# Optimization experiments

Measured on AMD Instinct MI355X. Metric: run time of the kernel, lower is better.

Reference implementation:

```python
import jax, jax.numpy as jnp
import numpy as np
from jax import lax

N = 1024          # n_ligand == n_receptor == feature dim (required by broadcast in source)
D = 1024          # gnn_input_dim == gnn_output_dim
H = 32            # hopi_output_dim
C = 32            # cnn_channels


def setup_inputs() -> dict:
    key = jax.random.key(0)
    ks = jax.random.split(key, 24)
    s = 0.02
    inp = {
        "ligand_node_features": jax.random.normal(ks[0], (N, D), jnp.float32),
        "ligand_edge_features": jax.random.normal(ks[1], (N, D), jnp.float32),
        "ligand_adjacency": jax.random.uniform(ks[2], (N, N), jnp.float32),
        "receptor_node_features": jax.random.normal(ks[3], (N, D), jnp.float32),
        "receptor_edge_features": jax.random.normal(ks[4], (N, D), jnp.float32),
        "receptor_adjacency": jax.random.uniform(ks[5], (N, N), jnp.float32),
        # GNNLayer params (shared between ligand and receptor, as in source)
        "Wn": jax.random.normal(ks[6], (D, D), jnp.float32) * s,
        "bn": jax.random.normal(ks[7], (D,), jnp.float32) * s,
        "We": jax.random.normal(ks[8], (D, D), jnp.float32) * s,
        "be": jax.random.normal(ks[9], (D,), jnp.float32) * s,
        "Wa": jax.random.normal(ks[10], (1, D), jnp.float32) * s,
        "ba": jax.random.normal(ks[11], (1,), jnp.float32) * s,
        # HighOrderPairwiseInteraction: Linear(2*D -> H)
        "W_hopi": jax.random.normal(ks[12], (H, 2 * D), jnp.float32) * s,
        "b_hopi": jax.random.normal(ks[13], (H,), jnp.float32) * s,
        # CNN tail
        "conv1_w": jax.random.normal(ks[14], (C, H, 3, 3), jnp.float32) * s,
        "conv1_b": jax.random.normal(ks[15], (C,), jnp.float32) * s,
        "conv2_w": jax.random.normal(ks[16], (C, C, 3, 3), jnp.float32) * s,
        "conv2_b": jax.random.normal(ks[17], (C,), jnp.float32) * s,
        "conv3_w": jax.random.normal(ks[18], (1, C, 1, 1), jnp.float32) * s,
        "conv3_b": jax.random.normal(ks[19], (1,), jnp.float32) * s,
    }
    return inp


def _gnn(nf, ef, Wn, bn, We, be, Wa, ba):
    # aggregated: [N, D]
    agg = jnp.tanh(nf @ Wn.T + bn + ef @ We.T + be)
    scores = agg @ Wa.T + ba                      # [N, 1]
    attn = jax.nn.softmax(scores, axis=1)         # softmax over size-1 dim -> ones (faithful)
    weighted = jnp.sum(agg * attn, axis=1)        # [N]
    return nf + weighted                          # [N,D] + [N] broadcasts over last dim (D == N)


def _conv(x, w, b):
    y = lax.conv_general_dilated(x, w, (1, 1), "SAME",
                                 dimension_numbers=("NCHW", "OIHW", "NCHW"))
    return y + b[None, :, None, None]


def reference(ligand_node_features, ligand_edge_features, ligand_adjacency,
              receptor_node_features, receptor_edge_features, receptor_adjacency,
              Wn, bn, We, be, Wa, ba, W_hopi, b_hopi,
              conv1_w, conv1_b, conv2_w, conv2_b, conv3_w, conv3_b):
    lig = _gnn(ligand_node_features, ligand_edge_features, Wn, bn, We, be, Wa, ba)
    rec = _gnn(receptor_node_features, receptor_edge_features, Wn, bn, We, be, Wa, ba)

    # HOPI: interactions[i, j] = Linear(cat(lig[i], rec[j])) == lig[i] @ Wl.T + rec[j] @ Wr.T + b
    Wl, Wr = W_hopi[:, :D], W_hopi[:, D:]
    lig_p = lig @ Wl.T                            # [N, H]
    rec_p = rec @ Wr.T                            # [N, H]
    interactions = lig_p[:, None, :] + rec_p[None, :, :] + b_hopi  # [N, N, H]

    x = jnp.transpose(interactions, (2, 0, 1))[None]  # [1, H, N, N]
    x = jax.nn.relu(_conv(x, conv1_w, conv1_b))
    x = jax.nn.relu(_conv(x, conv2_w, conv2_b))
    x = _conv(x, conv3_w, conv3_b)                # [1, 1, N, N]
    return x[0, 0]                                # [N, N]
```

## Files before the change

kernel.cpp:

```cpp
#include <hip/hip_runtime.h>


typedef _Float16 half8 __attribute__((ext_vector_type(8)));
typedef _Float16 half4 __attribute__((ext_vector_type(4)));
typedef float    f32x4 __attribute__((ext_vector_type(4)));

__device__ __forceinline__ short f2h_bits(float f){
    _Float16 h = (_Float16)f;
    return __builtin_bit_cast(short, h);
}
__device__ __forceinline__ half8 pack2(const float4& x, const float4& y){
    half8 r;
    r[0] = (_Float16)x.x; r[1] = (_Float16)x.y;
    r[2] = (_Float16)x.z; r[3] = (_Float16)x.w;
    r[4] = (_Float16)y.x; r[5] = (_Float16)y.y;
    r[6] = (_Float16)y.z; r[7] = (_Float16)y.w;
    return r;
}
__device__ __forceinline__ float tanh_fast(float x){
    float e = __expf(2.f * x);
    return 1.f - 2.f / (e + 1.f);
}

#define SWZ(c) ((((c) >> 1) & 3) << 3)

#define GNN_LOAD(AV, BV, KBN) {                                              \
    const int kbn_ = (KBN) & 2047;                                           \
    const float* Asrc_ = (kbn_ < 1024) ? A0 : A1;                            \
    const float* Bsrc_ = (kbn_ < 1024) ? Wn : We;                            \
    const int kk_ = kbn_ & 1023;                                             \
    const float* ap_ = Asrc_ + (size_t)(j0 + arow) * 1024 + kk_ + akc;       \
    const float* bp_ = Bsrc_ + (size_t)(d0 + brow) * 1024 + kk_ + bkc;       \
    AV[0] = *reinterpret_cast<const float4*>(ap_);                           \
    AV[1] = *reinterpret_cast<const float4*>(ap_ + 4);                       \
    AV[2] = *reinterpret_cast<const float4*>(ap_ + 8);                       \
    AV[3] = *reinterpret_cast<const float4*>(ap_ + 12);                      \
    BV[0] = *reinterpret_cast<const float4*>(bp_);                           \
    BV[1] = *reinterpret_cast<const float4*>(bp_ + 4);                       \
}

#define GNN_STAGE(AV, BV) {                                                  \
    const int ga_ = (t & 3) * 2;                                             \
    const int sa_ = arow & 7;                                                \
    *reinterpret_cast<half8*>(&As[arow * 64 + ((ga_    ) ^ sa_) * 8]) = pack2(AV[0], AV[1]); \
    *reinterpret_cast<half8*>(&As[arow * 64 + ((ga_ + 1) ^ sa_) * 8]) = pack2(AV[2], AV[3]); \
    *reinterpret_cast<half8*>(&Bs[brow * 64 + ((t & 7) ^ (brow & 7)) * 8]) = pack2(BV[0], BV[1]); \
}

#define GNN_MFMA() {                                                         \
    _Pragma("unroll")                                                        \
    for (int ks = 0; ks < 2; ++ks){                                          \
        half8 Af[2], Bf[2];                                                  \
        _Pragma("unroll")                                                    \
        for (int m = 0; m < 2; ++m){                                         \
            int row = wm * 32 + m * 16 + lr;                                 \
            int g   = ((ks * 4 + lg) ^ (row & 7)) * 8;                       \
            Af[m] = *reinterpret_cast<const half8*>(&As[row * 64 + g]);      \
        }                                                                    \
        _Pragma("unroll")                                                    \
        for (int n = 0; n < 2; ++n){                                         \
            int col = wn * 32 + n * 16 + lr;                                 \
            int g   = ((ks * 4 + lg) ^ (col & 7)) * 8;                       \
            Bf[n] = *reinterpret_cast<const half8*>(&Bs[col * 64 + g]);      \
        }                                                                    \
        _Pragma("unroll")                                                    \
        for (int m = 0; m < 2; ++m)                                          \
            _Pragma("unroll")                                                \
            for (int n = 0; n < 2; ++n)                                      \
                acc[m][n] = __builtin_amdgcn_mfma_f32_16x16x32_f16(          \
                    Af[m], Bf[n], acc[m][n], 0, 0, 0);                       \
    }                                                                        \
}

__global__ __launch_bounds__(512) void gnn_kernel(
    const float* __restrict__ lig_nf, const float* __restrict__ lig_ef,
    const float* __restrict__ rec_nf, const float* __restrict__ rec_ef,
    const float* __restrict__ Wn, const float* __restrict__ We,
    const float* __restrict__ bn, const float* __restrict__ be,
    float* __restrict__ part)
{
    __shared__ __attribute__((aligned(16))) short As[128 * 64];
    __shared__ __attribute__((aligned(16))) short Bs[64 * 64];
    __shared__ float red[128][2];

    const int t  = threadIdx.x;
    const int cx = blockIdx.z;
    const float* A0 = cx ? rec_nf : lig_nf;
    const float* A1 = cx ? rec_ef : lig_ef;
    const int j0 = blockIdx.x * 128;
    const int d0 = blockIdx.y * 64;

    const int wid  = t >> 6;
    const int wm   = wid >> 1;
    const int wn   = wid & 1;
    const int lane = t & 63;
    const int lr   = lane & 15;
    const int lg   = lane >> 4;

    f32x4 acc[2][2];
    #pragma unroll
    for (int m = 0; m < 2; ++m)
        #pragma unroll
        for (int n = 0; n < 2; ++n)
            acc[m][n] = (f32x4){0.f, 0.f, 0.f, 0.f};

    const int arow = t >> 2;
    const int akc  = (t & 3) * 16;
    const int brow = t >> 3;
    const int bkc  = (t & 7) * 8;

    float4 avA[4], bvA[2], avB[4], bvB[2];
    GNN_LOAD(avA, bvA, 0);
    GNN_LOAD(avB, bvB, 64);

    for (int kb = 0; kb < 2048; kb += 128){
        __syncthreads();
        GNN_STAGE(avA, bvA);
        GNN_LOAD(avA, bvA, kb + 128);
        __syncthreads();
        GNN_MFMA();
        __syncthreads();
        GNN_STAGE(avB, bvB);
        GNN_LOAD(avB, bvB, kb + 192);
        __syncthreads();
        GNN_MFMA();
    }

    float rowsum[2][4];
    #pragma unroll
    for (int m = 0; m < 2; ++m)
        #pragma unroll
        for (int jj = 0; jj < 4; ++jj) rowsum[m][jj] = 0.f;
    #pragma unroll
    for (int n = 0; n < 2; ++n){
        int d = d0 + wn * 32 + n * 16 + lr;
        float bias = bn[d] + be[d];
        #pragma unroll
        for (int m = 0; m < 2; ++m)
            #pragma unroll
            for (int jj = 0; jj < 4; ++jj)
                rowsum[m][jj] += tanh_fast(acc[m][n][jj] + bias);
    }
    #pragma unroll
    for (int mask = 1; mask < 16; mask <<= 1)
        #pragma unroll
        for (int m = 0; m < 2; ++m)
            #pragma unroll
            for (int jj = 0; jj < 4; ++jj)
                rowsum[m][jj] += __shfl_xor(rowsum[m][jj], mask);
    __syncthreads();
    if (lr == 0){
        #pragma unroll
        for (int m = 0; m < 2; ++m)
            #pragma unroll
            for (int jj = 0; jj < 4; ++jj)
                red[wm * 32 + m * 16 + lg * 4 + jj][wn] = rowsum[m][jj];
    }
    __syncthreads();
    if (t < 128)
        part[(size_t)cx * 16384 + (size_t)blockIdx.y * 1024 + j0 + t]
            = red[t][0] + red[t][1];
}

__global__ __launch_bounds__(256) void pp_kernel(
    const float* __restrict__ lig_nf, const float* __restrict__ rec_nf,
    const float* __restrict__ W_hopi, const float* __restrict__ b_hopi,
    const float* __restrict__ w1, const float* __restrict__ b1,
    const float* __restrict__ w2,
    const float* __restrict__ part,
    float* __restrict__ Kp, short* __restrict__ U16, short* __restrict__ V16,
    short* __restrict__ w2f16)
{
    __shared__ __attribute__((aligned(16))) char smem[46208];
    const int t = threadIdx.x;
    const int role = blockIdx.x;

    if (role < 32){
        short* As = reinterpret_cast<short*>(smem);
        short* Bs = reinterpret_cast<short*>(smem + 10240);
        short* Pz = reinterpret_cast<short*>(smem + 14336);
        short* Ws = reinterpret_cast<short*>(smem + 20736);

        const int cx = role >> 4;
        const int r0 = (role & 15) * 64;
        const float* nf = cx ? rec_nf : lig_nf;
        const float* W  = W_hopi + (cx ? 1024 : 0);
        short* O = cx ? V16 : U16;

        const int wid = t >> 6;
        const int lane = t & 63;
        const int lr = lane & 15;
        const int lg = lane >> 4;

        for (int e = t; e < 9216; e += 256){
            int cs  = e / 3072;
            int rem = e - cs * 3072;
            int co  = rem / 96;
            int k   = rem - co * 96;
            int d   = k >> 5;
            int ci  = k & 31;
            int o_lo = (cs == 1) ? 1 : 0;
            int o_hi = (cs == 2) ? 1 : 2;
            float s = 0.f;
            for (int o = o_lo; o <= o_hi; ++o){
                int tap = cx ? (o * 3 + d) : (d * 3 + o);
                s += w1[co * 288 + ci * 9 + tap];
            }
            Ws[(cs * 32 + co) * 104 + k] = f2h_bits(s);
        }

        f32x4 acc[2][2];
        #pragma unroll
        for (int mi = 0; mi < 2; ++mi)
            #pragma unroll
            for (int n = 0; n < 2; ++n)
                acc[mi][n] = (f32x4){0.f, 0.f, 0.f, 0.f};

        for (int kb = 0; kb < 16; ++kb){
            const int kcol = kb * 64;
            __syncthreads();
            for (int e = t; e < 320; e += 256){
                int rowl = e >> 2;
                int grow = r0 - 8 + rowl;
                int chunk = (e & 3) * 16;
                float4 a0, a1, a2, a3;
                if ((unsigned)grow < 1024u){
                    const float* ap = nf + (size_t)grow * 1024 + kcol + chunk;
                    a0 = *reinterpret_cast<const float4*>(ap);
                    a1 = *reinterpret_cast<const float4*>(ap + 4);
                    a2 = *reinterpret_cast<const float4*>(ap + 8);
                    a3 = *reinterpret_cast<const float4*>(ap + 12);
                } else {
                    a0 = a1 = a2 = a3 = make_float4(0.f, 0.f, 0.f, 0.f);
                }
                int ga = (e & 3) * 2;
                int sa = rowl & 7;
                *reinterpret_cast<half8*>(&As[rowl * 64 + ((ga    ) ^ sa) * 8]) = pack2(a0, a1);
                *reinterpret_cast<half8*>(&As[rowl * 64 + ((ga + 1) ^ sa) * 8]) = pack2(a2, a3);
            }
            {
                int row = t >> 3;
                int kc  = (t & 7) * 8;
                const float* bp = W + (size_t)row * 2048 + kcol + kc;
                float4 b0 = *reinterpret_cast<const float4*>(bp);
                float4 b1 = *reinterpret_cast<const float4*>(bp + 4);
                *reinterpret_cast<half8*>(&Bs[row * 64 + ((t & 7) ^ (row & 7)) * 8]) = pack2(b0, b1);
            }
            __syncthreads();
            #pragma unroll
            for (int mi = 0; mi < 2; ++mi){
                int mf = wid + mi * 4;
                if (mf >= 5) break;
                #pragma unroll
                for (int ks = 0; ks < 2; ++ks){
                    int ar = mf * 16 + lr;
                    half8 Af = *reinterpret_cast<const half8*>(
                        &As[ar * 64 + ((ks * 4 + lg) ^ (ar & 7)) * 8]);
                    #pragma unroll
                    for (int n = 0; n < 2; ++n){
                        int col = n * 16 + lr;
                        half8 Bf = *reinterpret_cast<const half8*>(
                            &Bs[col * 64 + ((ks * 4 + lg) ^ (col & 7)) * 8]);
                        acc[mi][n] = __builtin_amdgcn_mfma_f32_16x16x32_f16(
                            Af, Bf, acc[mi][n], 0, 0, 0);
                    }
                }
            }
        }
        #pragma unroll
        for (int mi = 0; mi < 2; ++mi){
            int mf = wid + mi * 4;
            if (mf >= 5) break;
            #pragma unroll
            for (int n = 0; n < 2; ++n)
                #pragma unroll
                for (int jj = 0; jj < 4; ++jj){
                    int rowl = mf * 16 + lg * 4 + jj;
                    Pz[rowl * 40 + n * 16 + lr] = f2h_bits(acc[mi][n][jj]);
                }
        }
        __syncthreads();

        f32x4 uacc[3][2];
        #pragma unroll
        for (int cs = 0; cs < 3; ++cs)
            #pragma unroll
            for (int n = 0; n < 2; ++n)
                uacc[cs][n] = (f32x4){0.f, 0.f, 0.f, 0.f};
        #pragma unroll
        for (int d = 0; d < 3; ++d){
            int ar = wid * 16 + lr;
            half8 Ap = *reinterpret_cast<const half8*>(
                &Pz[(7 + ar + d) * 40 + lg * 8]);
            #pragma unroll
            for (int cs = 0; cs < 3; ++cs)
                #pragma unroll
                for (int n = 0; n < 2; ++n){
                    half8 Bp = *reinterpret_cast<const half8*>(
                        &Ws[(cs * 32 + n * 16 + lr) * 104 + d * 32 + lg * 8]);
                    uacc[cs][n] = __builtin_amdgcn_mfma_f32_16x16x32_f16(
                        Ap, Bp, uacc[cs][n], 0, 0, 0);
                }
        }
        #pragma unroll
        for (int cs = 0; cs < 3; ++cs)
            #pragma unroll
            for (int n = 0; n < 2; ++n)
                #pragma unroll
                for (int jj = 0; jj < 4; ++jj){
                    int grow = r0 + wid * 16 + lg * 4 + jj;
                    O[((size_t)(cs << 10) + grow) * 32 + n * 16 + lr]
                        = f2h_bits(uacc[cs][n][jj]);
                }
        return;
    }

    if (role == 33){
        for (int e = t; e < 9216; e += 256){
            int co  = e / 288;
            int rem = e - co * 288;
            int ci  = rem / 9;
            int tap = rem - ci * 9;
            w2f16[(tap * 32 + co) * 32 + (ci ^ SWZ(co))] = f2h_bits(w2[e]);
        }
        return;
    }

    float* ws_l = reinterpret_cast<float*>(smem);
    float* ws_r = reinterpret_cast<float*>(smem + 4096);
    float* red  = reinterpret_cast<float*>(smem + 8192);
    float* cvs  = reinterpret_cast<float*>(smem + 9216);
    float* w1s  = reinterpret_cast<float*>(smem + 9344);

    #pragma unroll
    for (int q = 0; q < 9; ++q){
        int idx = (t + q * 256) * 4;
        *reinterpret_cast<float4*>(&w1s[idx]) =
            *reinterpret_cast<const float4*>(w1 + idx);
    }
    for (int j = t; j < 1024; j += 256){
        float sl = 0.f, sr = 0.f;
        #pragma unroll
        for (int b = 0; b < 16; ++b){
            sl += part[b * 1024 + j];
            sr += part[16384 + b * 1024 + j];
        }
        ws_l[j] = sl; ws_r[j] = sr;
    }
    __syncthreads();
    {
        const int h = t & 31;
        const int seg = t >> 5;
        const float* wl = W_hopi + (size_t)h * 2048 + seg * 128;
        const float* wr = wl + 1024;
        float s = 0.f;
        #pragma unroll 8
        for (int j = 0; j < 128; j += 4){
            float4 a = *reinterpret_cast<const float4*>(wl + j);
            float4 b = *reinterpret_cast<const float4*>(wr + j);
            const float* l = &ws_l[seg * 128 + j];
            const float* r = &ws_r[seg * 128 + j];
            s = fmaf(l[0], a.x, s); s = fmaf(l[1], a.y, s);
            s = fmaf(l[2], a.z, s); s = fmaf(l[3], a.w, s);
            s = fmaf(r[0], b.x, s); s = fmaf(r[1], b.y, s);
            s = fmaf(r[2], b.z, s); s = fmaf(r[3], b.w, s);
        }
        red[t] = s;
    }
    __syncthreads();
    if (t < 32){
        float tot = b_hopi[t];
        #pragma unroll
        for (int g = 0; g < 8; ++g) tot += red[g * 32 + t];
        cvs[t] = tot;
    }
    __syncthreads();
    for (int e = t; e < 288; e += 256){
        int co  = e & 31;
        int cse = e >> 5;
        int yc  = cse / 3, xc = cse - yc * 3;
        float sum = b1[co];
        for (int ci = 0; ci < 32; ++ci){
            const float* wp = &w1s[co * 288 + ci * 9];
            float t00 = wp[0], t01 = wp[1], t02 = wp[2];
            float t10 = wp[3], t11 = wp[4], t12 = wp[5];
            float t20 = wp[6], t21 = wp[7], t22 = wp[8];
            float r0, r1, r2;
            if (xc == 0){ r0 = t00+t01+t02; r1 = t10+t11+t12; r2 = t20+t21+t22; }
            else if (xc == 1){ r0 = t01+t02; r1 = t11+t12; r2 = t21+t22; }
            else { r0 = t00+t01; r1 = t10+t11; r2 = t20+t21; }
            float wsum = (yc == 0) ? (r0+r1+r2) : ((yc == 1) ? (r1+r2) : (r0+r1));
            sum = fmaf(cvs[ci], wsum, sum);
        }
        Kp[cse * 32 + co] = sum;
    }
}

__global__ __launch_bounds__(512) void conv_kernel(
    const short* __restrict__ U16, const short* __restrict__ V16,
    const float* __restrict__ Kp, const short* __restrict__ w2f16,
    const float* __restrict__ b2,
    const float* __restrict__ w3, const float* __restrict__ b3,
    float* __restrict__ outp)
{
    __shared__ __attribute__((aligned(16))) short ys[18 * 18 * 32];
    __shared__ __attribute__((aligned(16))) short wB[9 * 32 * 32];

    const int t    = threadIdx.x;
    const int oy0  = blockIdx.y * 16;
    const int ox0  = blockIdx.x * 16;
    const int wid  = t >> 6;
    const int lane = t & 63;
    const int lr   = lane & 15;
    const int lg   = lane >> 4;

    {
        const uint4* src = reinterpret_cast<const uint4*>(w2f16);
        uint4* dst = reinterpret_cast<uint4*>(wB);
        #pragma unroll
        for (int e = t; e < 1152; e += 512)
            dst[e] = src[e];
    }
    const bool interior = (blockIdx.x >= 1) & (blockIdx.x <= 62) &
                          (blockIdx.y >= 1) & (blockIdx.y <= 62);
    if (interior){
        const int cp = (t & 7) * 4;
        half4 k00;
        {
            float4 kf = *reinterpret_cast<const float4*>(&Kp[cp]);
            k00[0] = (_Float16)kf.x; k00[1] = (_Float16)kf.y;
            k00[2] = (_Float16)kf.z; k00[3] = (_Float16)kf.w;
        }
        #pragma unroll
        for (int pass = 0; pass < 6; ++pass){
            int idx = t + pass * 512;
            if (idx < 2592){
                int po  = idx >> 3;
                int ryo = po / 18;
                int rxo = po - ryo * 18;
                int gy = oy0 - 1 + ryo, gx = ox0 - 1 + rxo;
                half4 u = *reinterpret_cast<const half4*>(&U16[gy * 32 + cp]);
                half4 v = *reinterpret_cast<const half4*>(&V16[gx * 32 + cp]);
                half4 r = u + v + k00;
                #pragma unroll
                for (int e = 0; e < 4; ++e)
                    r[e] = r[e] > (_Float16)0.f ? r[e] : (_Float16)0.f;
                *reinterpret_cast<half4*>(&ys[po * 32 + (cp ^ SWZ(rxo))]) = r;
            }
        }
    } else {
        #pragma unroll
        for (int pass = 0; pass < 6; ++pass){
            int idx = t + pass * 512;
            if (idx < 2592){
                int po  = idx >> 3;
                int cp  = (idx & 7) * 4;
                int ryo = po / 18;
                int rxo = po - ryo * 18;
                int gy = oy0 - 1 + ryo, gx = ox0 - 1 + rxo;
                half4 h = {(_Float16)0.f, (_Float16)0.f, (_Float16)0.f, (_Float16)0.f};
                if ((unsigned)gy < 1024u && (unsigned)gx < 1024u){
                    int yc = (gy == 0) ? 1 : ((gy == 1023) ? 2 : 0);
                    int xc = (gx == 0) ? 1 : ((gx == 1023) ? 2 : 0);
                    half4 u = *reinterpret_cast<const half4*>(
                        &U16[((size_t)(xc << 10) + gy) * 32 + cp]);
                    half4 v = *reinterpret_cast<const half4*>(
                        &V16[((size_t)(yc << 10) + gx) * 32 + cp]);
                    float4 k = *reinterpret_cast<const float4*>(&Kp[(yc * 3 + xc) * 32 + cp]);
                    h[0] = (_Float16)fmaxf((float)u[0] + (float)v[0] + k.x, 0.f);
                    h[1] = (_Float16)fmaxf((float)u[1] + (float)v[1] + k.y, 0.f);
                    h[2] = (_Float16)fmaxf((float)u[2] + (float)v[2] + k.z, 0.f);
                    h[3] = (_Float16)fmaxf((float)u[3] + (float)v[3] + k.w, 0.f);
                }
                *reinterpret_cast<half4*>(&ys[po * 32 + (cp ^ SWZ(rxo))]) = h;
            }
        }
    }
    __syncthreads();

    {
        half8 Bf[2][9];
        float bias[2], w3v[2];
        #pragma unroll
        for (int n = 0; n < 2; ++n){
            int co = n * 16 + lr;
            bias[n] = b2[co];
            w3v[n]  = w3[co];
            #pragma unroll
            for (int tap = 0; tap < 9; ++tap)
                Bf[n][tap] = *reinterpret_cast<const half8*>(
                    &wB[(tap * 32 + co) * 32 + ((lg * 8) ^ SWZ(co))]);
        }
        const float b3v = b3[0];
        for (int s = wid; s < 16; s += 8){
            int p  = s * 16 + lr;
            int ry = p >> 4;
            int rx = p & 15;
            f32x4 acc0 = {0.f, 0.f, 0.f, 0.f};
            f32x4 acc1 = {0.f, 0.f, 0.f, 0.f};
            #pragma unroll
            for (int tap = 0; tap < 9; ++tap){
                const int dy = tap / 3, dx = tap - (tap / 3) * 3;
                int pix = (ry + dy) * 18 + rx + dx;
                half8 A = *reinterpret_cast<const half8*>(
                    &ys[pix * 32 + ((lg * 8) ^ SWZ(rx + dx))]);
                acc0 = __builtin_amdgcn_mfma_f32_16x16x32_f16(A, Bf[0][tap], acc0, 0, 0, 0);
                acc1 = __builtin_amdgcn_mfma_f32_16x16x32_f16(A, Bf[1][tap], acc1, 0, 0, 0);
            }
            float part[4];
            #pragma unroll
            for (int j = 0; j < 4; ++j)
                part[j] = w3v[0] * fmaxf(acc0[j] + bias[0], 0.f)
                        + w3v[1] * fmaxf(acc1[j] + bias[1], 0.f);
            #pragma unroll
            for (int m = 1; m < 16; m <<= 1)
                #pragma unroll
                for (int j = 0; j < 4; ++j)
                    part[j] += __shfl_xor(part[j], m);
            if (lr == 0){
                float4 o = make_float4(part[0] + b3v, part[1] + b3v,
                                       part[2] + b3v, part[3] + b3v);
                *reinterpret_cast<float4*>(outp + (size_t)(oy0 + s) * 1024 + ox0 + lg * 4) = o;
            }
        }
    }
}

extern "C" void kernel_launch(void* const* d_in, const int* in_sizes, int n_in,
                              void* d_out, int out_size, void* d_ws, size_t ws_size,
                              hipStream_t stream)
{
    const float* lig_nf = (const float*)d_in[0];
    const float* lig_ef = (const float*)d_in[1];
    const float* rec_nf = (const float*)d_in[3];
    const float* rec_ef = (const float*)d_in[4];
    const float* Wn     = (const float*)d_in[6];
    const float* bn     = (const float*)d_in[7];
    const float* We     = (const float*)d_in[8];
    const float* be     = (const float*)d_in[9];
    const float* W_hopi = (const float*)d_in[12];
    const float* b_hopi = (const float*)d_in[13];
    const float* w1     = (const float*)d_in[14];
    const float* b1     = (const float*)d_in[15];
    const float* w2     = (const float*)d_in[16];
    const float* b2     = (const float*)d_in[17];
    const float* w3     = (const float*)d_in[18];
    const float* b3     = (const float*)d_in[19];
    float* outp = (float*)d_out;

    float* part  = (float*)d_ws;
    float* Kp    = (float*)((char*)d_ws + 393216);
    short* U16   = (short*)((char*)d_ws + 394368);
    short* V16   = (short*)((char*)d_ws + 590976);
    short* w2f16 = (short*)((char*)d_ws + 787584);

    dim3 g1(8, 16, 2);
    gnn_kernel<<<g1, 512, 0, stream>>>(lig_nf, lig_ef, rec_nf, rec_ef,
                                       Wn, We, bn, be, part);
    pp_kernel<<<34, 256, 0, stream>>>(lig_nf, rec_nf, W_hopi, b_hopi,
                                      w1, b1, w2, part, Kp, U16, V16, w2f16);
    dim3 g3(64, 64);
    conv_kernel<<<g3, 512, 0, stream>>>(U16, V16, Kp, w2f16, b2, w3, b3, outp);
}
```

Baseline: 117.9 us.

## Double-buffer register prefetch in pp_kernel and widen blocks to 512 threads

Rewrites the HOPI projection GEMM in pp_kernel so global loads for the next two K-tiles go into registers while the current tile is staged to LDS and multiplied. The block grows from 256 to 512 threads so each of 5 waves owns one 16-row M fragment instead of waves looping over two. The other roles are adjusted for the new thread count. This aims to hide global load latency in a small 34-block kernel, at the cost of more registers and extra barriers per K step.

New measurement: 114.9 us. 2.5% less time.

```diff
diff --git a/kernel.cpp b/kernel.cpp
--- a/kernel.cpp
+++ b/kernel.cpp
@@ -15,6 +15,12 @@
     r[2] = (_Float16)x.z; r[3] = (_Float16)x.w;
     r[4] = (_Float16)y.x; r[5] = (_Float16)y.y;
     r[6] = (_Float16)y.z; r[7] = (_Float16)y.w;
+    return r;
+}
+__device__ __forceinline__ half4 pack4(const float4& x){
+    half4 r;
+    r[0] = (_Float16)x.x; r[1] = (_Float16)x.y;
+    r[2] = (_Float16)x.z; r[3] = (_Float16)x.w;
     return r;
 }
 __device__ __forceinline__ float tanh_fast(float x){
@@ -162,7 +168,66 @@
             = red[t][0] + red[t][1];
 }
 
-__global__ __launch_bounds__(256) void pp_kernel(
+#define PP_LOAD(AV, BV, KBN) {                                               \
+    const int kcol_ = (KBN) & 1023;                                          \
+    _Pragma("unroll")                                                        \
+    for (int p = 0; p < 3; ++p){                                             \
+        int e_ = t + 512 * p;                                                \
+        if (e_ < 1280){                                                      \
+            int rowl_ = e_ >> 4;                                             \
+            int grow_ = r0 - 8 + rowl_;                                      \
+            if ((unsigned)grow_ < 1024u)                                     \
+                AV[p] = *reinterpret_cast<const float4*>(                    \
+                    nf + (size_t)grow_ * 1024 + kcol_ + (e_ & 15) * 4);      \
+            else                                                             \
+                AV[p] = make_float4(0.f, 0.f, 0.f, 0.f);                     \
+        }                                                                    \
+    }                                                                        \
+    BV = *reinterpret_cast<const float4*>(                                   \
+        W + (size_t)(t >> 4) * 2048 + kcol_ + (t & 15) * 4);                 \
+}
+
+#define PP_STAGE(AV, BV) {                                                   \
+    _Pragma("unroll")                                                        \
+    for (int p = 0; p < 3; ++p){                                             \
+        int e_ = t + 512 * p;                                                \
+        if (e_ < 1280){                                                      \
+            int rowl_ = e_ >> 4;                                             \
+            int ga_ = (e_ & 15) >> 1;                                        \
+            int sub_ = (e_ & 1) * 4;                                         \
+            *reinterpret_cast<half4*>(                                       \
+                &As[rowl_ * 64 + ((ga_ ^ (rowl_ & 7)) * 8) + sub_]) = pack4(AV[p]); \
+        }                                                                    \
+    }                                                                        \
+    {                                                                        \
+        int row_ = t >> 4;                                                   \
+        int ga_ = (t & 15) >> 1;                                             \
+        int sub_ = (t & 1) * 4;                                              \
+        *reinterpret_cast<half4*>(                                           \
+            &Bs[row_ * 64 + ((ga_ ^ (row_ & 7)) * 8) + sub_]) = pack4(BV);   \
+    }                                                                        \
+}
+
+#define PP_MFMA() {                                                          \
+    if (wid < 5){                                                            \
+        _Pragma("unroll")                                                    \
+        for (int ks = 0; ks < 2; ++ks){                                      \
+            int ar_ = wid * 16 + lr;                                         \
+            half8 Af = *reinterpret_cast<const half8*>(                      \
+                &As[ar_ * 64 + ((ks * 4 + lg) ^ (ar_ & 7)) * 8]);            \
+            _Pragma("unroll")                                                \
+            for (int n = 0; n < 2; ++n){                                     \
+                int col_ = n * 16 + lr;                                      \
+                half8 Bf = *reinterpret_cast<const half8*>(                  \
+                    &Bs[col_ * 64 + ((ks * 4 + lg) ^ (col_ & 7)) * 8]);      \
+                pacc[n] = __builtin_amdgcn_mfma_f32_16x16x32_f16(            \
+                    Af, Bf, pacc[n], 0, 0, 0);                               \
+            }                                                                \
+        }                                                                    \
+    }                                                                        \
+}
+
+__global__ __launch_bounds__(512) void pp_kernel(
     const float* __restrict__ lig_nf, const float* __restrict__ rec_nf,
     const float* __restrict__ W_hopi, const float* __restrict__ b_hopi,
     const float* __restrict__ w1, const float* __restrict__ b1,
@@ -171,7 +236,7 @@
     float* __restrict__ Kp, short* __restrict__ U16, short* __restrict__ V16,
     short* __restrict__ w2f16)
 {
-    __shared__ __attribute__((aligned(16))) char smem[46208];
+    __shared__ __attribute__((aligned(16))) char smem[47232];
     const int t = threadIdx.x;
     const int role = blockIdx.x;
 
@@ -192,7 +257,7 @@
         const int lr = lane & 15;
         const int lg = lane >> 4;
 
-        for (int e = t; e < 9216; e += 256){
+        for (int e = t; e < 9216; e += 512){
             int cs  = e / 3072;
             int rem = e - cs * 3072;
             int co  = rem / 96;
@@ -209,114 +274,77 @@
             Ws[(cs * 32 + co) * 104 + k] = f2h_bits(s);
         }
 
-        f32x4 acc[2][2];
-        #pragma unroll
-        for (int mi = 0; mi < 2; ++mi)
-            #pragma unroll
-            for (int n = 0; n < 2; ++n)
-                acc[mi][n] = (f32x4){0.f, 0.f, 0.f, 0.f};
-
-        for (int kb = 0; kb < 16; ++kb){
-            const int kcol = kb * 64;
+        f32x4 pacc[2];
+        pacc[0] = (f32x4){0.f, 0.f, 0.f, 0.f};
+        pacc[1] = (f32x4){0.f, 0.f, 0.f, 0.f};
+
+        float4 avA[3], avB[3];
+        float4 bvA, bvB;
+        PP_LOAD(avA, bvA, 0);
+        PP_LOAD(avB, bvB, 64);
+
+        for (int kb = 0; kb < 1024; kb += 128){
             __syncthreads();
-            for (int e = t; e < 320; e += 256){
-                int rowl = e >> 2;
-                int grow = r0 - 8 + rowl;
-                int chunk = (e & 3) * 16;
-                float4 a0, a1, a2, a3;
-                if ((unsigned)grow < 1024u){
-                    const float* ap = nf + (size_t)grow * 1024 + kcol + chunk;
-                    a0 = *reinterpret_cast<const float4*>(ap);
-                    a1 = *reinterpret_cast<const float4*>(ap + 4);
-                    a2 = *reinterpret_cast<const float4*>(ap + 8);
-                    a3 = *reinterpret_cast<const float4*>(ap + 12);
-                } else {
-                    a0 = a1 = a2 = a3 = make_float4(0.f, 0.f, 0.f, 0.f);
-                }
-                int ga = (e & 3) * 2;
-                int sa = rowl & 7;
-                *reinterpret_cast<half8*>(&As[rowl * 64 + ((ga    ) ^ sa) * 8]) = pack2(a0, a1);
-                *reinterpret_cast<half8*>(&As[rowl * 64 + ((ga + 1) ^ sa) * 8]) = pack2(a2, a3);
-            }
-            {
-                int row = t >> 3;
-                int kc  = (t & 7) * 8;
-                const float* bp = W + (size_t)row * 2048 + kcol + kc;
-                float4 b0 = *reinterpret_cast<const float4*>(bp);
-                float4 b1 = *reinterpret_cast<const float4*>(bp + 4);
-                *reinterpret_cast<half8*>(&Bs[row * 64 + ((t & 7) ^ (row & 7)) * 8]) = pack2(b0, b1);
-            }
+            PP_STAGE(avA, bvA);
+            PP_LOAD(avA, bvA, kb + 128);
             __syncthreads();
-            #pragma unroll
-            for (int mi = 0; mi < 2; ++mi){
-                int mf = wid + mi * 4;
-                if (mf >= 5) break;
-                #pragma unroll
-                for (int ks = 0; ks < 2; ++ks){
-                    int ar = mf * 16 + lr;
-                    half8 Af = *reinterpret_cast<const half8*>(
-                        &As[ar * 64 + ((ks * 4 + lg) ^ (ar & 7)) * 8]);
-                    #pragma unroll
-                    for (int n = 0; n < 2; ++n){
-                        int col = n * 16 + lr;
-                        half8 Bf = *reinterpret_cast<const half8*>(
-                            &Bs[col * 64 + ((ks * 4 + lg) ^ (col & 7)) * 8]);
-                        acc[mi][n] = __builtin_amdgcn_mfma_f32_16x16x32_f16(
-                            Af, Bf, acc[mi][n], 0, 0, 0);
-                    }
-                }
-            }
-        }
-        #pragma unroll
-        for (int mi = 0; mi < 2; ++mi){
-            int mf = wid + mi * 4;
-            if (mf >= 5) break;
+            PP_MFMA();
+            __syncthreads();
+            PP_STAGE(avB, bvB);
+            PP_LOAD(avB, bvB, kb + 192);
+            __syncthreads();
+            PP_MFMA();
+        }
+
+        if (wid < 5){
             #pragma unroll
             for (int n = 0; n < 2; ++n)
                 #pragma unroll
                 for (int jj = 0; jj < 4; ++jj){
-                    int rowl = mf * 16 + lg * 4 + jj;
-                    Pz[rowl * 40 + n * 16 + lr] = f2h_bits(acc[mi][n][jj]);
+                    int rowl = wid * 16 + lg * 4 + jj;
+                    Pz[rowl * 40 + n * 16 + lr] = f2h_bits(pacc[n][jj]);
                 }
         }
         __syncthreads();
 
-        f32x4 uacc[3][2];
-        #pragma unroll
-        for (int cs = 0; cs < 3; ++cs)
-            #pragma unroll
-            for (int n = 0; n < 2; ++n)
-                uacc[cs][n] = (f32x4){0.f, 0.f, 0.f, 0.f};
-        #pragma unroll
-        for (int d = 0; d < 3; ++d){
-            int ar = wid * 16 + lr;
-            half8 Ap = *reinterpret_cast<const half8*>(
-                &Pz[(7 + ar + d) * 40 + lg * 8]);
+        if (wid < 4){
+            f32x4 uacc[3][2];
             #pragma unroll
             for (int cs = 0; cs < 3; ++cs)
                 #pragma unroll
-                for (int n = 0; n < 2; ++n){
-                    half8 Bp = *reinterpret_cast<const half8*>(
-                        &Ws[(cs * 32 + n * 16 + lr) * 104 + d * 32 + lg * 8]);
-                    uacc[cs][n] = __builtin_amdgcn_mfma_f32_16x16x32_f16(
-                        Ap, Bp, uacc[cs][n], 0, 0, 0);
-                }
-        }
-        #pragma unroll
-        for (int cs = 0; cs < 3; ++cs)
-            #pragma unroll
-            for (int n = 0; n < 2; ++n)
+                for (int n = 0; n < 2; ++n)
+                    uacc[cs][n] = (f32x4){0.f, 0.f, 0.f, 0.f};
+            #pragma unroll
+            for (int d = 0; d < 3; ++d){
+                int ar = wid * 16 + lr;
+                half8 Ap = *reinterpret_cast<const half8*>(
+                    &Pz[(7 + ar + d) * 40 + lg * 8]);
                 #pragma unroll
-                for (int jj = 0; jj < 4; ++jj){
-                    int grow = r0 + wid * 16 + lg * 4 + jj;
-                    O[((size_t)(cs << 10) + grow) * 32 + n * 16 + lr]
-                        = f2h_bits(uacc[cs][n][jj]);
-                }
+                for (int cs = 0; cs < 3; ++cs)
+                    #pragma unroll
+                    for (int n = 0; n < 2; ++n){
+                        half8 Bp = *reinterpret_cast<const half8*>(
+                            &Ws[(cs * 32 + n * 16 + lr) * 104 + d * 32 + lg * 8]);
+                        uacc[cs][n] = __builtin_amdgcn_mfma_f32_16x16x32_f16(
+                            Ap, Bp, uacc[cs][n], 0, 0, 0);
+                    }
+            }
+            #pragma unroll
+            for (int cs = 0; cs < 3; ++cs)
+                #pragma unroll
+                for (int n = 0; n < 2; ++n)
+                    #pragma unroll
+                    for (int jj = 0; jj < 4; ++jj){
+                        int grow = r0 + wid * 16 + lg * 4 + jj;
+                        O[((size_t)(cs << 10) + grow) * 32 + n * 16 + lr]
+                            = f2h_bits(uacc[cs][n][jj]);
+                    }
+        }
         return;
     }
 
     if (role == 33){
-        for (int e = t; e < 9216; e += 256){
+        for (int e = t; e < 9216; e += 512){
             int co  = e / 288;
             int rem = e - co * 288;
             int ci  = rem / 9;
@@ -329,16 +357,17 @@
     float* ws_l = reinterpret_cast<float*>(smem);
     float* ws_r = reinterpret_cast<float*>(smem + 4096);
     float* red  = reinterpret_cast<float*>(smem + 8192);
-    float* cvs  = reinterpret_cast<float*>(smem + 9216);
-    float* w1s  = reinterpret_cast<float*>(smem + 9344);
+    float* cvs  = reinterpret_cast<float*>(smem + 10240);
+    float* w1s  = reinterpret_cast<float*>(smem + 10368);
 
     #pragma unroll
-    for (int q = 0; q < 9; ++q){
-        int idx = (t + q * 256) * 4;
-        *reinterpret_cast<float4*>(&w1s[idx]) =
-            *reinterpret_cast<const float4*>(w1 + idx);
-    }
-    for (int j = t; j < 1024; j += 256){
+    for (int q = 0; q < 5; ++q){
+        int i4 = t + q * 512;
+        if (i4 < 2304)
+            *reinterpret_cast<float4*>(&w1s[i4 * 4]) =
+                *reinterpret_cast<const float4*>(w1 + i4 * 4);
+    }
+    for (int j = t; j < 1024; j += 512){
         float sl = 0.f, sr = 0.f;
         #pragma unroll
         for (int b = 0; b < 16; ++b){
@@ -351,15 +380,15 @@
     {
         const int h = t & 31;
         const int seg = t >> 5;
-        const float* wl = W_hopi + (size_t)h * 2048 + seg * 128;
+        const float* wl = W_hopi + (size_t)h * 2048 + seg * 64;
         const float* wr = wl + 1024;
         float s = 0.f;
         #pragma unroll 8
-        for (int j = 0; j < 128; j += 4){
+        for (int j = 0; j < 64; j += 4){
             float4 a = *reinterpret_cast<const float4*>(wl + j);
             float4 b = *reinterpret_cast<const float4*>(wr + j);
-            const float* l = &ws_l[seg * 128 + j];
-            const float* r = &ws_r[seg * 128 + j];
+            const float* l = &ws_l[seg * 64 + j];
+            const float* r = &ws_r[seg * 64 + j];
             s = fmaf(l[0], a.x, s); s = fmaf(l[1], a.y, s);
             s = fmaf(l[2], a.z, s); s = fmaf(l[3], a.w, s);
             s = fmaf(r[0], b.x, s); s = fmaf(r[1], b.y, s);
@@ -371,11 +400,11 @@
     if (t < 32){
         float tot = b_hopi[t];
         #pragma unroll
-        for (int g = 0; g < 8; ++g) tot += red[g * 32 + t];
+        for (int g = 0; g < 16; ++g) tot += red[g * 32 + t];
         cvs[t] = tot;
     }
     __syncthreads();
-    for (int e = t; e < 288; e += 256){
+    for (int e = t; e < 288; e += 512){
         int co  = e & 31;
         int cse = e >> 5;
         int yc  = cse / 3, xc = cse - yc * 3;
@@ -557,7 +586,7 @@
     dim3 g1(8, 16, 2);
     gnn_kernel<<<g1, 512, 0, stream>>>(lig_nf, lig_ef, rec_nf, rec_ef,
                                        Wn, We, bn, be, part);
-    pp_kernel<<<34, 256, 0, stream>>>(lig_nf, rec_nf, W_hopi, b_hopi,
+    pp_kernel<<<34, 512, 0, stream>>>(lig_nf, rec_nf, W_hopi, b_hopi,
                                       w1, b1, w2, part, Kp, U16, V16, w2f16);
     dim3 g3(64, 64);
     conv_kernel<<<g3, 512, 0, stream>>>(U16, V16, Kp, w2f16, b2, w3, b3, outp);
```
